# Optimization experiments

Measured on AMD Instinct MI355X. Metric: run time of the kernel, lower is better.

Reference implementation:

```python
import jax, jax.numpy as jnp
import numpy as np

# config (matches cfg init_kwargs)
FG_THRESH = 0.5
BG_THRESH_LO = 0.1
BG_THRESH_HI = 0.5
N_FG_ROIS = 128
N_ROIS = 512
MEAN = np.array([0.0, 0.0, 0.0, 0.0], dtype=np.float32)
STD = np.array([0.2, 0.2, 0.2, 0.2], dtype=np.float32)

N_PROP = 262144
N_GT = 128


def _make_boxes(key, n, img=1024.0):
    k1, k2 = jax.random.split(key)
    xy = jax.random.uniform(k1, (n, 2), dtype=jnp.float32) * (img - 64.0)
    wh = jax.random.uniform(k2, (n, 2), dtype=jnp.float32) * 192.0 + 8.0
    return jnp.concatenate([xy, xy + wh], axis=-1)  # [n,4] valid x1y1x2y2


def setup_inputs() -> dict:
    key = jax.random.key(0)
    k1, k2, k3 = jax.random.split(key, 3)
    rois = _make_boxes(k1, N_PROP)[None]          # [1, N, 4]
    gt_bbox = _make_boxes(k2, N_GT)[None]         # [1, G, 4]
    labels = jax.random.randint(k3, (1, N_GT), 0, 81, dtype=jnp.int32)  # [1, G]
    return {"rois": rois, "gt_bbox": gt_bbox, "labels": labels}


def _iou_matrix(boxes, gt):
    # boxes [M,4], gt [G,4] -> [M,G] IoU with +1 pixel convention
    bx1, by1, bx2, by2 = boxes[:, 0:1], boxes[:, 1:2], boxes[:, 2:3], boxes[:, 3:4]
    gx1, gy1, gx2, gy2 = gt[None, :, 0], gt[None, :, 1], gt[None, :, 2], gt[None, :, 3]
    iw = jnp.clip(jnp.minimum(bx2, gx2) - jnp.maximum(bx1, gx1) + 1.0, 0.0)
    ih = jnp.clip(jnp.minimum(by2, gy2) - jnp.maximum(by1, gy1) + 1.0, 0.0)
    inter = iw * ih
    area_b = (bx2 - bx1 + 1.0) * (by2 - by1 + 1.0)          # [M,1]
    area_g = (gx2 - gx1 + 1.0) * (gy2 - gy1 + 1.0)          # [1,G]
    return inter / (area_b + area_g - inter)


def _bbox_transform(rois, gt):
    w = rois[:, 2] - rois[:, 0] + 1.0
    h = rois[:, 3] - rois[:, 1] + 1.0
    cx = rois[:, 0] + 0.5 * w
    cy = rois[:, 1] + 0.5 * h
    gw = gt[:, 2] - gt[:, 0] + 1.0
    gh = gt[:, 3] - gt[:, 1] + 1.0
    gcx = gt[:, 0] + 0.5 * gw
    gcy = gt[:, 1] + 0.5 * gh
    return jnp.stack([(gcx - cx) / w, (gcy - cy) / h,
                      jnp.log(gw / w), jnp.log(gh / h)], axis=1)


def _forward(rois, gt_bbox, labels):
    rois = rois[0]          # [N,4]
    gt = gt_bbox[0]         # [G,4]
    lab = labels[0]         # [G]
    all_rois = jnp.concatenate([rois, gt], axis=0)          # [M,4], M=N+G
    ious = _iou_matrix(all_rois, gt)                        # [M,G]  <- dominant traffic
    argmax_row = jnp.argmax(ious, axis=1)                   # [M]
    max_row = jnp.max(ious, axis=1)                         # [M]

    fg = max_row > FG_THRESH
    bg = (max_row > BG_THRESH_LO) & (max_row < BG_THRESH_HI)

    # fixed-size, deterministic variant of the fg/bg sampling:
    # keep first min(N_FG_ROIS, #fg) fg, then fill with bg up to N_ROIS
    fg_cum = jnp.cumsum(fg.astype(jnp.int32))
    sel_fg = fg & (fg_cum <= N_FG_ROIS)
    n_fg = jnp.minimum(N_FG_ROIS, fg_cum[-1])
    bg_cum = jnp.cumsum(bg.astype(jnp.int32))
    sel_bg = bg & (bg_cum <= (N_ROIS - n_fg))

    # stable sort key: fg first (0), then bg (1), then padding rows (2)
    key = jnp.where(sel_fg, 0, jnp.where(sel_bg, 1, 2)).astype(jnp.int32)
    order = jnp.argsort(key, stable=True)
    idx = order[:N_ROIS]                                    # [N_ROIS]

    rois_out = jnp.take(all_rois, idx, axis=0)              # [N_ROIS,4]
    gt_idx = jnp.take(argmax_row, idx)
    labels_out = jnp.take(lab, gt_idx)                      # [N_ROIS]
    gt_out = jnp.take(gt, gt_idx, axis=0)

    delta = _bbox_transform(rois_out, gt_out)
    delta = (delta - jnp.asarray(MEAN)) / jnp.asarray(STD)  # intended normalization
    return rois_out, delta, labels_out


def reference(rois, gt_bbox, labels):
    return _forward(rois, gt_bbox, labels)
```

## Files before the change

### kernel.cpp

```cpp
#include <hip/hip_runtime.h>
#include <stdint.h>

#define N_PROP    262144
#define N_GT      128
#define N_ALL     (N_PROP + N_GT)
#define NFG_MAX   128
#define NROIS_OUT 512
#define BLK       256
#define NBLOCKS   ((N_ALL + BLK - 1) / BLK)

#define OFF_PACKED 0
#define OFF_CNT    524544

__global__ __launch_bounds__(BLK) void k_iou(
    const float* __restrict__ rois, const float* __restrict__ gt,
    uint16_t* __restrict__ packed, uint32_t* __restrict__ cnt)
{
    __shared__ float sga[N_GT];
    int tid = threadIdx.x;
    if (tid < N_GT) {
        float4 g = *reinterpret_cast<const float4*>(gt + 4 * tid);
        sga[tid] = __fmul_rn(__fadd_rn(__fsub_rn(g.z, g.x), 1.0f),
                             __fadd_rn(__fsub_rn(g.w, g.y), 1.0f));
    }
    __syncthreads();

    int i = blockIdx.x * BLK + tid;
    bool v = (i < N_ALL);
    float4 b = {0, 0, 0, 0};
    if (v) {
        const float* p = (i < N_PROP) ? (rois + 4 * (size_t)i)
                                      : (gt + 4 * (size_t)(i - N_PROP));
        b = *reinterpret_cast<const float4*>(p);
    }
    float a = __fmul_rn(__fadd_rn(__fsub_rn(b.z, b.x), 1.0f),
                        __fadd_rn(__fsub_rn(b.w, b.y), 1.0f));

    float best = -1.0f; int bestj = 0;
    if (v) {
        #pragma unroll 4
        for (int j = 0; j < N_GT; ++j) {
            float gx = gt[4 * j + 0];
            float gy = gt[4 * j + 1];
            float gz = gt[4 * j + 2];
            float gw = gt[4 * j + 3];
            float ga = sga[j];
            float iw = fmaxf(__fadd_rn(__fsub_rn(fminf(b.z, gz), fmaxf(b.x, gx)), 1.0f), 0.0f);
            float ih = fmaxf(__fadd_rn(__fsub_rn(fminf(b.w, gw), fmaxf(b.y, gy)), 1.0f), 0.0f);
            float inter = __fmul_rn(iw, ih);
            float denom = __fsub_rn(__fadd_rn(a, ga), inter);
            float iou = __fdiv_rn(inter, denom);
            if (iou > best) { best = iou; bestj = j; }
        }
    }
    bool fg = v && (best > 0.5f);
    bool bg = v && (best > 0.1f) && (best < 0.5f);
    if (v) {
        int flagv = fg ? 0 : (bg ? 1 : 2);
        packed[i] = (uint16_t)((flagv << 8) | bestj);
    }
    unsigned long long mf = __ballot(fg ? 1 : 0);
    unsigned long long mb = __ballot(bg ? 1 : 0);
    __shared__ int sF[BLK / 64], sB[BLK / 64];
    int lane = tid & 63, w = tid >> 6;
    if (lane == 0) { sF[w] = __popcll(mf); sB[w] = __popcll(mb); }
    __syncthreads();
    if (tid == 0) {
        int tf = 0, tb = 0;
        for (int k = 0; k < BLK / 64; ++k) { tf += sF[k]; tb += sB[k]; }
        cnt[blockIdx.x] = ((uint32_t)tb << 16) | (uint32_t)tf;
    }
}

__global__ __launch_bounds__(BLK) void k_select(
    const float* __restrict__ rois, const float* __restrict__ gt,
    const int* __restrict__ labels,
    const uint16_t* __restrict__ packed, const uint32_t* __restrict__ cnt,
    float* __restrict__ out)
{
    int tid = threadIdx.x, bid = blockIdx.x;
    int i = bid * BLK + tid;
    bool valid = (i < N_ALL);
    uint16_t p = valid ? packed[i] : (uint16_t)(2 << 8);
    int flagv = p >> 8;
    int g = p & 0xFF;
    bool isfg = valid && (flagv == 0);
    bool isbg = valid && (flagv == 1);

    int totF = 0, totB = 0, preF = 0, preB = 0;
    for (int j = tid; j < NBLOCKS; j += BLK) {
        uint32_t c = cnt[j];
        int f = (int)(c & 0xFFFFu), bb = (int)(c >> 16);
        totF += f; totB += bb;
        if (j < bid) { preF += f; preB += bb; }
    }
    #pragma unroll
    for (int off = 32; off > 0; off >>= 1) {
        totF += __shfl_down(totF, off, 64);
        totB += __shfl_down(totB, off, 64);
        preF += __shfl_down(preF, off, 64);
        preB += __shfl_down(preB, off, 64);
    }
    __shared__ int sTF[4], sTB[4], sPF[4], sPB[4];
    __shared__ int sWF[4], sWB[4];
    int lane = tid & 63, w = tid >> 6;
    if (lane == 0) { sTF[w] = totF; sTB[w] = totB; sPF[w] = preF; sPB[w] = preB; }

    unsigned long long mf = __ballot(isfg ? 1 : 0);
    unsigned long long mb = __ballot(isbg ? 1 : 0);
    unsigned long long lemask = (lane == 63) ? ~0ull : ((1ull << (lane + 1)) - 1ull);
    int inclF = __popcll(mf & lemask);
    int inclB = __popcll(mb & lemask);
    if (lane == 0) { sWF[w] = __popcll(mf); sWB[w] = __popcll(mb); }
    __syncthreads();

    totF = sTF[0] + sTF[1] + sTF[2] + sTF[3];
    totB = sTB[0] + sTB[1] + sTB[2] + sTB[3];
    preF = sPF[0] + sPF[1] + sPF[2] + sPF[3];
    preB = sPB[0] + sPB[1] + sPB[2] + sPB[3];
    int wPreF = 0, wPreB = 0;
    for (int k = 0; k < 4; ++k) {
        if (k < w) { wPreF += sWF[k]; wPreB += sWB[k]; }
    }
    if (!valid) return;

    int NF  = totF < NFG_MAX ? totF : NFG_MAX;
    int LIM = NROIS_OUT - NF;
    int NB  = totB < LIM ? totB : LIM;

    int fgCum = preF + wPreF + inclF;
    int bgCum = preB + wPreB + inclB;

    int pos;
    if (isfg && fgCum <= NFG_MAX) {
        pos = fgCum - 1;
    } else if (isbg && bgCum <= LIM) {
        pos = NF + bgCum - 1;
    } else {
        int selF = fgCum < NFG_MAX ? fgCum : NFG_MAX;
        int selB = bgCum < LIM ? bgCum : LIM;
        int restCum = (i + 1) - selF - selB;
        pos = NF + NB + restCum - 1;
    }
    if (pos >= NROIS_OUT) return;

    const float* rp = (i < N_PROP) ? (rois + 4 * (size_t)i)
                                   : (gt + 4 * (size_t)(i - N_PROP));
    float4 r = *reinterpret_cast<const float4*>(rp);
    float4 gb = *reinterpret_cast<const float4*>(gt + 4 * (size_t)g);

    float wdt = __fadd_rn(__fsub_rn(r.z, r.x), 1.0f);
    float hgt = __fadd_rn(__fsub_rn(r.w, r.y), 1.0f);
    float cx  = __fadd_rn(r.x, __fmul_rn(0.5f, wdt));
    float cy  = __fadd_rn(r.y, __fmul_rn(0.5f, hgt));
    float gw  = __fadd_rn(__fsub_rn(gb.z, gb.x), 1.0f);
    float gh  = __fadd_rn(__fsub_rn(gb.w, gb.y), 1.0f);
    float gcx = __fadd_rn(gb.x, __fmul_rn(0.5f, gw));
    float gcy = __fadd_rn(gb.y, __fmul_rn(0.5f, gh));

    float d0 = __fdiv_rn(__fdiv_rn(__fsub_rn(gcx, cx), wdt), 0.2f);
    float d1 = __fdiv_rn(__fdiv_rn(__fsub_rn(gcy, cy), hgt), 0.2f);
    float d2 = __fdiv_rn(logf(__fdiv_rn(gw, wdt)), 0.2f);
    float d3 = __fdiv_rn(logf(__fdiv_rn(gh, hgt)), 0.2f);

    out[4 * pos + 0] = r.x;
    out[4 * pos + 1] = r.y;
    out[4 * pos + 2] = r.z;
    out[4 * pos + 3] = r.w;
    out[2048 + 4 * pos + 0] = d0;
    out[2048 + 4 * pos + 1] = d1;
    out[2048 + 4 * pos + 2] = d2;
    out[2048 + 4 * pos + 3] = d3;
    out[4096 + pos] = (float)labels[g];
}

extern "C" void kernel_launch(void* const* d_in, const int* in_sizes, int n_in,
                              void* d_out, int out_size, void* d_ws, size_t ws_size,
                              hipStream_t stream)
{
    const float* rois   = (const float*)d_in[0];
    const float* gt     = (const float*)d_in[1];
    const int*   labels = (const int*)d_in[2];
    float* out = (float*)d_out;

    char* ws = (char*)d_ws;
    uint16_t* packed = (uint16_t*)(ws + OFF_PACKED);
    uint32_t* cnt    = (uint32_t*)(ws + OFF_CNT);

    k_iou<<<NBLOCKS, BLK, 0, stream>>>(rois, gt, packed, cnt);
    k_select<<<NBLOCKS, BLK, 0, stream>>>(rois, gt, labels, packed, cnt, out);
}
```

Measured before the change: 40.19 us.

## Fuse IoU and selection kernels via cooperative grid sync

Merges the IoU/argmax kernel and the selection/regression kernel into one cooperative kernel that uses a grid-wide sync between the per-block count phase and the prefix/scatter phase. Each thread keeps its box, best IoU and argmax in registers, so the packed intermediate buffer and the second read of the rois are no longer needed. The GT loop is also changed to load float4 GT boxes and float4 areas, four per iteration. The cost is a grid barrier across all 1025 blocks. It also requires every block to be co-resident, or the cooperative launch fails.

Result: slower. 144.8 us (+260.4%).

```diff
diff --git a/kernel.cpp b/kernel.cpp
--- a/kernel.cpp
+++ b/kernel.cpp
@@ -1,5 +1,8 @@
 #include <hip/hip_runtime.h>
+#include <hip/hip_cooperative_groups.h>
 #include <stdint.h>
+
+namespace cg = cooperative_groups;
 
 #define N_PROP    262144
 #define N_GT      128
@@ -9,15 +12,29 @@
 #define BLK       256
 #define NBLOCKS   ((N_ALL + BLK - 1) / BLK)
 
-#define OFF_PACKED 0
-#define OFF_CNT    524544
+#define OFF_CNT 0
 
-__global__ __launch_bounds__(BLK) void k_iou(
+#define IOU_STEP(gv, gav, jidx)                                                        \
+    {                                                                                  \
+        float iw = fmaxf(__fadd_rn(__fsub_rn(fminf(b.z, (gv).z), fmaxf(b.x, (gv).x)), 1.0f), 0.0f); \
+        float ih = fmaxf(__fadd_rn(__fsub_rn(fminf(b.w, (gv).w), fmaxf(b.y, (gv).y)), 1.0f), 0.0f); \
+        float inter = __fmul_rn(iw, ih);                                               \
+        float denom = __fsub_rn(__fadd_rn(a, (gav)), inter);                           \
+        float iou = __fdiv_rn(inter, denom);                                           \
+        if (iou > best) { best = iou; bestj = (jidx); }                                \
+    }
+
+__global__ __launch_bounds__(BLK) void k_fused(
     const float* __restrict__ rois, const float* __restrict__ gt,
-    uint16_t* __restrict__ packed, uint32_t* __restrict__ cnt)
+    const int* __restrict__ labels, uint32_t* __restrict__ cnt,
+    float* __restrict__ out)
 {
     __shared__ float sga[N_GT];
-    int tid = threadIdx.x;
+    __shared__ int sF[4], sB[4];
+    __shared__ int sTF[4], sTB[4], sPF[4], sPB[4], sWF[4], sWB[4];
+    int tid = threadIdx.x, bid = blockIdx.x;
+    int lane = tid & 63, w = tid >> 6;
+
     if (tid < N_GT) {
         float4 g = *reinterpret_cast<const float4*>(gt + 4 * tid);
         sga[tid] = __fmul_rn(__fadd_rn(__fsub_rn(g.z, g.x), 1.0f),
@@ -25,9 +42,9 @@
     }
     __syncthreads();
 
-    int i = blockIdx.x * BLK + tid;
+    int i = bid * BLK + tid;
     bool v = (i < N_ALL);
-    float4 b = {0, 0, 0, 0};
+    float4 b = {0.f, 0.f, 0.f, 0.f};
     if (v) {
         const float* p = (i < N_PROP) ? (rois + 4 * (size_t)i)
                                       : (gt + 4 * (size_t)(i - N_PROP));
@@ -37,55 +54,34 @@
                         __fadd_rn(__fsub_rn(b.w, b.y), 1.0f));
 
     float best = -1.0f; int bestj = 0;
-    if (v) {
-        #pragma unroll 4
-        for (int j = 0; j < N_GT; ++j) {
-            float gx = gt[4 * j + 0];
-            float gy = gt[4 * j + 1];
-            float gz = gt[4 * j + 2];
-            float gw = gt[4 * j + 3];
-            float ga = sga[j];
-            float iw = fmaxf(__fadd_rn(__fsub_rn(fminf(b.z, gz), fmaxf(b.x, gx)), 1.0f), 0.0f);
-            float ih = fmaxf(__fadd_rn(__fsub_rn(fminf(b.w, gw), fmaxf(b.y, gy)), 1.0f), 0.0f);
-            float inter = __fmul_rn(iw, ih);
-            float denom = __fsub_rn(__fadd_rn(a, ga), inter);
-            float iou = __fdiv_rn(inter, denom);
-            if (iou > best) { best = iou; bestj = j; }
-        }
+    const float4* gtv  = reinterpret_cast<const float4*>(gt);
+    const float4* sgaV = reinterpret_cast<const float4*>(sga);
+    #pragma unroll 2
+    for (int jj = 0; jj < N_GT / 4; ++jj) {
+        float4 ga4 = sgaV[jj];
+        float4 g0 = gtv[4 * jj + 0];
+        float4 g1 = gtv[4 * jj + 1];
+        float4 g2 = gtv[4 * jj + 2];
+        float4 g3 = gtv[4 * jj + 3];
+        IOU_STEP(g0, ga4.x, 4 * jj + 0);
+        IOU_STEP(g1, ga4.y, 4 * jj + 1);
+        IOU_STEP(g2, ga4.z, 4 * jj + 2);
+        IOU_STEP(g3, ga4.w, 4 * jj + 3);
     }
+
     bool fg = v && (best > 0.5f);
     bool bg = v && (best > 0.1f) && (best < 0.5f);
-    if (v) {
-        int flagv = fg ? 0 : (bg ? 1 : 2);
-        packed[i] = (uint16_t)((flagv << 8) | bestj);
-    }
+
     unsigned long long mf = __ballot(fg ? 1 : 0);
     unsigned long long mb = __ballot(bg ? 1 : 0);
-    __shared__ int sF[BLK / 64], sB[BLK / 64];
-    int lane = tid & 63, w = tid >> 6;
     if (lane == 0) { sF[w] = __popcll(mf); sB[w] = __popcll(mb); }
     __syncthreads();
-    if (tid == 0) {
-        int tf = 0, tb = 0;
-        for (int k = 0; k < BLK / 64; ++k) { tf += sF[k]; tb += sB[k]; }
-        cnt[blockIdx.x] = ((uint32_t)tb << 16) | (uint32_t)tf;
-    }
-}
+    if (tid == 0)
+        cnt[bid] = ((uint32_t)(sB[0] + sB[1] + sB[2] + sB[3]) << 16)
+                 |  (uint32_t)(sF[0] + sF[1] + sF[2] + sF[3]);
 
-__global__ __launch_bounds__(BLK) void k_select(
-    const float* __restrict__ rois, const float* __restrict__ gt,
-    const int* __restrict__ labels,
-    const uint16_t* __restrict__ packed, const uint32_t* __restrict__ cnt,
-    float* __restrict__ out)
-{
-    int tid = threadIdx.x, bid = blockIdx.x;
-    int i = bid * BLK + tid;
-    bool valid = (i < N_ALL);
-    uint16_t p = valid ? packed[i] : (uint16_t)(2 << 8);
-    int flagv = p >> 8;
-    int g = p & 0xFF;
-    bool isfg = valid && (flagv == 0);
-    bool isbg = valid && (flagv == 1);
+    __threadfence();
+    cg::this_grid().sync();
 
     int totF = 0, totB = 0, preF = 0, preB = 0;
     for (int j = tid; j < NBLOCKS; j += BLK) {
@@ -101,17 +97,14 @@
         preF += __shfl_down(preF, off, 64);
         preB += __shfl_down(preB, off, 64);
     }
-    __shared__ int sTF[4], sTB[4], sPF[4], sPB[4];
-    __shared__ int sWF[4], sWB[4];
-    int lane = tid & 63, w = tid >> 6;
     if (lane == 0) { sTF[w] = totF; sTB[w] = totB; sPF[w] = preF; sPB[w] = preB; }
 
-    unsigned long long mf = __ballot(isfg ? 1 : 0);
-    unsigned long long mb = __ballot(isbg ? 1 : 0);
+    unsigned long long mf2 = __ballot(fg ? 1 : 0);
+    unsigned long long mb2 = __ballot(bg ? 1 : 0);
     unsigned long long lemask = (lane == 63) ? ~0ull : ((1ull << (lane + 1)) - 1ull);
-    int inclF = __popcll(mf & lemask);
-    int inclB = __popcll(mb & lemask);
-    if (lane == 0) { sWF[w] = __popcll(mf); sWB[w] = __popcll(mb); }
+    int inclF = __popcll(mf2 & lemask);
+    int inclB = __popcll(mb2 & lemask);
+    if (lane == 0) { sWF[w] = __popcll(mf2); sWB[w] = __popcll(mb2); }
     __syncthreads();
 
     totF = sTF[0] + sTF[1] + sTF[2] + sTF[3];
@@ -122,7 +115,7 @@
     for (int k = 0; k < 4; ++k) {
         if (k < w) { wPreF += sWF[k]; wPreB += sWB[k]; }
     }
-    if (!valid) return;
+    if (!v) return;
 
     int NF  = totF < NFG_MAX ? totF : NFG_MAX;
     int LIM = NROIS_OUT - NF;
@@ -132,9 +125,9 @@
     int bgCum = preB + wPreB + inclB;
 
     int pos;
-    if (isfg && fgCum <= NFG_MAX) {
+    if (fg && fgCum <= NFG_MAX) {
         pos = fgCum - 1;
-    } else if (isbg && bgCum <= LIM) {
+    } else if (bg && bgCum <= LIM) {
         pos = NF + bgCum - 1;
     } else {
         int selF = fgCum < NFG_MAX ? fgCum : NFG_MAX;
@@ -144,15 +137,12 @@
     }
     if (pos >= NROIS_OUT) return;
 
-    const float* rp = (i < N_PROP) ? (rois + 4 * (size_t)i)
-                                   : (gt + 4 * (size_t)(i - N_PROP));
-    float4 r = *reinterpret_cast<const float4*>(rp);
-    float4 gb = *reinterpret_cast<const float4*>(gt + 4 * (size_t)g);
+    float4 gb = gtv[bestj];
 
-    float wdt = __fadd_rn(__fsub_rn(r.z, r.x), 1.0f);
-    float hgt = __fadd_rn(__fsub_rn(r.w, r.y), 1.0f);
-    float cx  = __fadd_rn(r.x, __fmul_rn(0.5f, wdt));
-    float cy  = __fadd_rn(r.y, __fmul_rn(0.5f, hgt));
+    float wdt = __fadd_rn(__fsub_rn(b.z, b.x), 1.0f);
+    float hgt = __fadd_rn(__fsub_rn(b.w, b.y), 1.0f);
+    float cx  = __fadd_rn(b.x, __fmul_rn(0.5f, wdt));
+    float cy  = __fadd_rn(b.y, __fmul_rn(0.5f, hgt));
     float gw  = __fadd_rn(__fsub_rn(gb.z, gb.x), 1.0f);
     float gh  = __fadd_rn(__fsub_rn(gb.w, gb.y), 1.0f);
     float gcx = __fadd_rn(gb.x, __fmul_rn(0.5f, gw));
@@ -163,15 +153,15 @@
     float d2 = __fdiv_rn(logf(__fdiv_rn(gw, wdt)), 0.2f);
     float d3 = __fdiv_rn(logf(__fdiv_rn(gh, hgt)), 0.2f);
 
-    out[4 * pos + 0] = r.x;
-    out[4 * pos + 1] = r.y;
-    out[4 * pos + 2] = r.z;
-    out[4 * pos + 3] = r.w;
+    out[4 * pos + 0] = b.x;
+    out[4 * pos + 1] = b.y;
+    out[4 * pos + 2] = b.z;
+    out[4 * pos + 3] = b.w;
     out[2048 + 4 * pos + 0] = d0;
     out[2048 + 4 * pos + 1] = d1;
     out[2048 + 4 * pos + 2] = d2;
     out[2048 + 4 * pos + 3] = d3;
-    out[4096 + pos] = (float)labels[g];
+    out[4096 + pos] = (float)labels[bestj];
 }
 
 extern "C" void kernel_launch(void* const* d_in, const int* in_sizes, int n_in,
@@ -182,11 +172,9 @@
     const float* gt     = (const float*)d_in[1];
     const int*   labels = (const int*)d_in[2];
     float* out = (float*)d_out;
+    uint32_t* cnt = (uint32_t*)((char*)d_ws + OFF_CNT);
 
-    char* ws = (char*)d_ws;
-    uint16_t* packed = (uint16_t*)(ws + OFF_PACKED);
-    uint32_t* cnt    = (uint32_t*)(ws + OFF_CNT);
-
-    k_iou<<<NBLOCKS, BLK, 0, stream>>>(rois, gt, packed, cnt);
-    k_select<<<NBLOCKS, BLK, 0, stream>>>(rois, gt, labels, packed, cnt, out);
+    void* args[] = { (void*)&rois, (void*)&gt, (void*)&labels, (void*)&cnt, (void*)&out };
+    hipLaunchCooperativeKernel((const void*)k_fused, dim3(NBLOCKS), dim3(BLK),
+                               args, 0, stream);
 }
```

## Split GT loop across two threads per ROI and vectorize GT loads

Applied to the files above, without the earlier changes.

Each IoU block now handles 128 boxes with 256 threads. Two threads share one box, each scanning half of the 128 GT boxes, and the two results are merged through shared memory. GT coordinates and areas are read as float4 vectors, and the select kernel adjusts its prefix scan to twice as many count entries. This halves the serial divide-heavy loop per thread and doubles the number of waves. The cost is an extra block barrier, shared-memory traffic, and a larger count array to scan in the select kernel.

New measurement: 39.78 us. About the same (-1.0%).

```diff
diff --git a/kernel.cpp b/kernel.cpp
--- a/kernel.cpp
+++ b/kernel.cpp
@@ -7,17 +7,37 @@
 #define NFG_MAX   128
 #define NROIS_OUT 512
 #define BLK       256
-#define NBLOCKS   ((N_ALL + BLK - 1) / BLK)
+#define ITEMS1    128
+#define NB1       (N_ALL / ITEMS1)
+#define NCNT      NB1
+#define NB2       ((N_ALL + BLK - 1) / BLK)
 
 #define OFF_PACKED 0
 #define OFF_CNT    524544
+
+#define IOU_STEP(gv, gav, jidx)                                                        \
+    {                                                                                  \
+        float iw = fmaxf(__fadd_rn(__fsub_rn(fminf(b.z, (gv).z), fmaxf(b.x, (gv).x)), 1.0f), 0.0f); \
+        float ih = fmaxf(__fadd_rn(__fsub_rn(fminf(b.w, (gv).w), fmaxf(b.y, (gv).y)), 1.0f), 0.0f); \
+        float inter = __fmul_rn(iw, ih);                                               \
+        float denom = __fsub_rn(__fadd_rn(a, (gav)), inter);                           \
+        float iou = __fdiv_rn(inter, denom);                                           \
+        if (iou > best) { best = iou; bestj = (jidx); }                                \
+    }
 
 __global__ __launch_bounds__(BLK) void k_iou(
     const float* __restrict__ rois, const float* __restrict__ gt,
     uint16_t* __restrict__ packed, uint32_t* __restrict__ cnt)
 {
     __shared__ float sga[N_GT];
+    __shared__ float sBest[ITEMS1];
+    __shared__ int   sBj[ITEMS1];
+    __shared__ int   sF[2], sB[2];
+
     int tid = threadIdx.x;
+    int half = tid >> 7;
+    int li   = tid & 127;
+
     if (tid < N_GT) {
         float4 g = *reinterpret_cast<const float4*>(gt + 4 * tid);
         sga[tid] = __fmul_rn(__fadd_rn(__fsub_rn(g.z, g.x), 1.0f),
@@ -25,51 +45,51 @@
     }
     __syncthreads();
 
-    int i = blockIdx.x * BLK + tid;
-    bool v = (i < N_ALL);
-    float4 b = {0, 0, 0, 0};
-    if (v) {
-        const float* p = (i < N_PROP) ? (rois + 4 * (size_t)i)
-                                      : (gt + 4 * (size_t)(i - N_PROP));
-        b = *reinterpret_cast<const float4*>(p);
-    }
+    int i = blockIdx.x * ITEMS1 + li;
+    const float* p = (i < N_PROP) ? (rois + 4 * (size_t)i)
+                                  : (gt + 4 * (size_t)(i - N_PROP));
+    float4 b = *reinterpret_cast<const float4*>(p);
     float a = __fmul_rn(__fadd_rn(__fsub_rn(b.z, b.x), 1.0f),
                         __fadd_rn(__fsub_rn(b.w, b.y), 1.0f));
 
-    float best = -1.0f; int bestj = 0;
-    if (v) {
-        #pragma unroll 4
-        for (int j = 0; j < N_GT; ++j) {
-            float gx = gt[4 * j + 0];
-            float gy = gt[4 * j + 1];
-            float gz = gt[4 * j + 2];
-            float gw = gt[4 * j + 3];
-            float ga = sga[j];
-            float iw = fmaxf(__fadd_rn(__fsub_rn(fminf(b.z, gz), fmaxf(b.x, gx)), 1.0f), 0.0f);
-            float ih = fmaxf(__fadd_rn(__fsub_rn(fminf(b.w, gw), fmaxf(b.y, gy)), 1.0f), 0.0f);
-            float inter = __fmul_rn(iw, ih);
-            float denom = __fsub_rn(__fadd_rn(a, ga), inter);
-            float iou = __fdiv_rn(inter, denom);
-            if (iou > best) { best = iou; bestj = j; }
-        }
-    }
-    bool fg = v && (best > 0.5f);
-    bool bg = v && (best > 0.1f) && (best < 0.5f);
-    if (v) {
-        int flagv = fg ? 0 : (bg ? 1 : 2);
-        packed[i] = (uint16_t)((flagv << 8) | bestj);
-    }
-    unsigned long long mf = __ballot(fg ? 1 : 0);
-    unsigned long long mb = __ballot(bg ? 1 : 0);
-    __shared__ int sF[BLK / 64], sB[BLK / 64];
-    int lane = tid & 63, w = tid >> 6;
-    if (lane == 0) { sF[w] = __popcll(mf); sB[w] = __popcll(mb); }
-    __syncthreads();
-    if (tid == 0) {
-        int tf = 0, tb = 0;
-        for (int k = 0; k < BLK / 64; ++k) { tf += sF[k]; tb += sB[k]; }
-        cnt[blockIdx.x] = ((uint32_t)tb << 16) | (uint32_t)tf;
-    }
+    float best = -1.0f; int bestj = half * 64;
+    const float4* gtv  = reinterpret_cast<const float4*>(gt);
+    const float4* sgaV = reinterpret_cast<const float4*>(sga);
+    int jjBase = half * 16;
+    #pragma unroll 2
+    for (int jj = 0; jj < 16; ++jj) {
+        int jg = jjBase + jj;
+        float4 ga4 = sgaV[jg];
+        float4 g0 = gtv[4 * jg + 0];
+        float4 g1 = gtv[4 * jg + 1];
+        float4 g2 = gtv[4 * jg + 2];
+        float4 g3 = gtv[4 * jg + 3];
+        IOU_STEP(g0, ga4.x, 4 * jg + 0);
+        IOU_STEP(g1, ga4.y, 4 * jg + 1);
+        IOU_STEP(g2, ga4.z, 4 * jg + 2);
+        IOU_STEP(g3, ga4.w, 4 * jg + 3);
+    }
+
+    if (half) { sBest[li] = best; sBj[li] = bestj; }
+    __syncthreads();
+
+    if (!half) {
+        float bh = sBest[li]; int jh = sBj[li];
+        if (bh > best) { best = bh; bestj = jh; }
+
+        bool fg = best > 0.5f;
+        bool bg = (best > 0.1f) && (best < 0.5f);
+        packed[i] = (uint16_t)(((fg ? 0 : (bg ? 1 : 2)) << 8) | bestj);
+
+        unsigned long long mf = __ballot(fg ? 1 : 0);
+        unsigned long long mb = __ballot(bg ? 1 : 0);
+        int lane = tid & 63, w = tid >> 6;
+        if (lane == 0) { sF[w] = __popcll(mf); sB[w] = __popcll(mb); }
+    }
+    __syncthreads();
+    if (tid == 0)
+        cnt[blockIdx.x] = ((uint32_t)(sB[0] + sB[1]) << 16)
+                        |  (uint32_t)(sF[0] + sF[1]);
 }
 
 __global__ __launch_bounds__(BLK) void k_select(
@@ -88,11 +108,11 @@
     bool isbg = valid && (flagv == 1);
 
     int totF = 0, totB = 0, preF = 0, preB = 0;
-    for (int j = tid; j < NBLOCKS; j += BLK) {
+    for (int j = tid; j < NCNT; j += BLK) {
         uint32_t c = cnt[j];
         int f = (int)(c & 0xFFFFu), bb = (int)(c >> 16);
         totF += f; totB += bb;
-        if (j < bid) { preF += f; preB += bb; }
+        if (j < 2 * bid) { preF += f; preB += bb; }
     }
     #pragma unroll
     for (int off = 32; off > 0; off >>= 1) {
@@ -187,6 +207,6 @@
     uint16_t* packed = (uint16_t*)(ws + OFF_PACKED);
     uint32_t* cnt    = (uint32_t*)(ws + OFF_CNT);
 
-    k_iou<<<NBLOCKS, BLK, 0, stream>>>(rois, gt, packed, cnt);
-    k_select<<<NBLOCKS, BLK, 0, stream>>>(rois, gt, labels, packed, cnt, out);
+    k_iou<<<NB1, BLK, 0, stream>>>(rois, gt, packed, cnt);
+    k_select<<<NB2, BLK, 0, stream>>>(rois, gt, labels, packed, cnt, out);
 }
```
